# Performance work log

Hardware: AMD Instinct MI355X
Metric: run time of the kernel (lower is better)

The kernel has to match this reference:

```python
import jax, jax.numpy as jnp
import numpy as np

BETA = 0.025
K, D = 8192, 256
B, T = 32, 1024

def setup_inputs() -> dict:
    key = jax.random.key(0)
    k1, k2 = jax.random.split(key)
    z_e = jax.random.normal(k1, (B, T, D), dtype=jnp.float32)
    # variance_scaling(scale=1, mode='fan_avg', distribution='uniform') over (K, D)
    fan_avg = (K + D) / 2.0
    limit = np.sqrt(3.0 / fan_avg)
    codebook = jax.random.uniform(k2, (K, D), dtype=jnp.float32, minval=-limit, maxval=limit)
    return {"z_e": z_e, "codebook": codebook}

def reference(z_e, codebook):
    flat = z_e.reshape(-1, D)  # [N, D]
    x_sqr = jnp.sum(flat ** 2, axis=-1, keepdims=True)        # [N, 1]
    c_sqr = jnp.sum(codebook ** 2, axis=-1)[None, :]           # [1, K]
    distances = x_sqr - 2.0 * (flat @ codebook.T) + c_sqr      # [N, K]
    encoding_indices = jnp.argmin(distances, axis=-1).reshape(z_e.shape[:-1])  # [B, T]
    quantize = codebook[encoding_indices]                      # [B, T, D]
    encoding_loss = jnp.mean((jax.lax.stop_gradient(z_e) - quantize) ** 2)
    commitment_loss = jnp.mean((z_e - jax.lax.stop_gradient(quantize)) ** 2)
    loss = encoding_loss + BETA * commitment_loss
    z_q = z_e + jax.lax.stop_gradient(quantize - z_e)          # straight-through
    return (z_q, encoding_indices, loss)
```

## Files before the change

kernel.cpp:

```cpp
#include <hip/hip_runtime.h>

#define D     256
#define K     8192
#define NROWS 32768
#define BETA  0.025f
#define TAU_NEW 4e-4f
#define TAU_OLD 2e-4f

typedef __bf16 bf16x8 __attribute__((ext_vector_type(8)));
typedef unsigned short ushort8v __attribute__((ext_vector_type(8)));
typedef float f32x16 __attribute__((ext_vector_type(16)));

#define MFMA(a,b,c) __builtin_amdgcn_mfma_f32_32x32x16_bf16(a,b,c,0,0,0)

typedef __attribute__((address_space(3))) unsigned int lds_uint;
typedef __attribute__((address_space(1))) unsigned int glb_uint;
__device__ __forceinline__ void gld16(const void* g, void* l) {
    __builtin_amdgcn_global_load_lds((const glb_uint*)g, (lds_uint*)l, 16, 0, 0);
}

__device__ __forceinline__ unsigned short bf_rn(float x) {
    unsigned u = __float_as_uint(x);
    return (unsigned short)((u + 0x7FFFu + ((u >> 16) & 1u)) >> 16);
}
__device__ __forceinline__ void split2(float x, unsigned short& h, unsigned short& l) {
    h = bf_rn(x);
    float hf = __uint_as_float(((unsigned)h) << 16);
    l = bf_rn(x - hf);
}

__global__ __launch_bounds__(256)
void np_sumsq_kernel(const float* __restrict__ src, float* __restrict__ dst,
                     int nrows) {
    const int tid  = threadIdx.x;
    const int w    = tid >> 6;
    const int lane = tid & 63;
    const int row  = blockIdx.x * 4 + w;
    if (row >= nrows) return;
    const float* a = src + (size_t)row * D;
    float r = 0.0f;
    if (lane < 16) {
        const float* h = a + (lane >> 3) * 128;
        const int j = lane & 7;
        float v = h[j];
        r = __fmul_rn(v, v);
        #pragma unroll
        for (int i = 8; i < 128; i += 8) {
            float u = h[i + j];
            r = __fadd_rn(r, __fmul_rn(u, u));
        }
    }
    float rr[16];
    #pragma unroll
    for (int t = 0; t < 16; ++t) rr[t] = __shfl(r, t, 64);
    if (lane == 0) {
        float h0 = __fadd_rn(__fadd_rn(__fadd_rn(rr[0], rr[1]), __fadd_rn(rr[2], rr[3])),
                             __fadd_rn(__fadd_rn(rr[4], rr[5]), __fadd_rn(rr[6], rr[7])));
        float h1 = __fadd_rn(__fadd_rn(__fadd_rn(rr[8], rr[9]), __fadd_rn(rr[10], rr[11])),
                             __fadd_rn(__fadd_rn(rr[12], rr[13]), __fadd_rn(rr[14], rr[15])));
        dst[row] = __fadd_rn(h0, h1);
    }
}

__global__ __launch_bounds__(64)
void np_sumsq_flagged_kernel(const float* __restrict__ ze,
                             const int* __restrict__ nflag,
                             const int* __restrict__ flags,
                             float* __restrict__ x2, int cap) {
    const int lane = threadIdx.x;
    const int nf   = min(nflag[0], cap);
    for (int f = blockIdx.x; f < nf; f += gridDim.x) {
        const int row = flags[f];
        const float* a = ze + (size_t)row * D;
        float r = 0.0f;
        if (lane < 16) {
            const float* h = a + (lane >> 3) * 128;
            const int j = lane & 7;
            float v = h[j];
            r = __fmul_rn(v, v);
            #pragma unroll
            for (int i = 8; i < 128; i += 8) {
                float u = h[i + j];
                r = __fadd_rn(r, __fmul_rn(u, u));
            }
        }
        float rr[16];
        #pragma unroll
        for (int t = 0; t < 16; ++t) rr[t] = __shfl(r, t, 64);
        if (lane == 0) {
            float h0 = __fadd_rn(__fadd_rn(__fadd_rn(rr[0], rr[1]), __fadd_rn(rr[2], rr[3])),
                                 __fadd_rn(__fadd_rn(rr[4], rr[5]), __fadd_rn(rr[6], rr[7])));
            float h1 = __fadd_rn(__fadd_rn(__fadd_rn(rr[8], rr[9]), __fadd_rn(rr[10], rr[11])),
                                 __fadd_rn(__fadd_rn(rr[12], rr[13]), __fadd_rn(rr[14], rr[15])));
            x2[row] = __fadd_rn(h0, h1);
        }
    }
}

__global__ __launch_bounds__(256)
void pack_cb_kernel(const float* __restrict__ cb, unsigned short* __restrict__ cbp) {
    const int t  = blockIdx.x;
    const int l  = threadIdx.x & 63;
    const int cq = threadIdx.x >> 6;
    const int row = t * 32 + (l & 31);
    const int db  = 8 * (l >> 5);
    #pragma unroll
    for (int ci = 0; ci < 4; ++ci) {
        const int c  = cq * 4 + ci;
        const int d0 = c * 16 + db;
        float4 v0 = *reinterpret_cast<const float4*>(&cb[(size_t)row * D + d0]);
        float4 v1 = *reinterpret_cast<const float4*>(&cb[(size_t)row * D + d0 + 4]);
        float xv[8] = {v0.x, v0.y, v0.z, v0.w, v1.x, v1.y, v1.z, v1.w};
        ushort8v uh, ul;
        #pragma unroll
        for (int j = 0; j < 8; ++j) {
            unsigned short hh, ll;
            split2(xv[j], hh, ll);
            uh[j] = hh; ul[j] = ll;
        }
        *reinterpret_cast<ushort8v*>(cbp + (size_t)t * 16384 + (c * 2 + 0) * 512 + l * 8) = uh;
        *reinterpret_cast<ushort8v*>(cbp + (size_t)t * 16384 + (c * 2 + 1) * 512 + l * 8) = ul;
    }
}

__global__ __attribute__((amdgpu_waves_per_eu(2, 2))) __launch_bounds__(256)
void mfma_argmin_kernel(const float* __restrict__ ze,
                        const unsigned short* __restrict__ cbp,
                        const float* __restrict__ c2,
                        float2* __restrict__ tops, int* __restrict__ topi) {
    __shared__ unsigned short lds[2 * 16384];
    const int tid = threadIdx.x;
    const int l   = tid & 63;
    const int w   = tid >> 6;
    const int ks  = blockIdx.x & 1;
    const int nb  = blockIdx.x >> 1;
    const int n   = nb * 128 + w * 32 + (l & 31);
    const int h   = l >> 5;

    bf16x8 Bh[16], Bl[16];
    {
        const float* zr = ze + (size_t)n * D + 8 * h;
        #pragma unroll
        for (int c = 0; c < 16; ++c) {
            float4 v0 = *reinterpret_cast<const float4*>(zr + c * 16);
            float4 v1 = *reinterpret_cast<const float4*>(zr + c * 16 + 4);
            float xv[8] = {v0.x, v0.y, v0.z, v0.w, v1.x, v1.y, v1.z, v1.w};
            ushort8v uh, ul;
            #pragma unroll
            for (int j = 0; j < 8; ++j) {
                unsigned short hh, ll;
                split2(xv[j], hh, ll);
                uh[j] = hh; ul[j] = ll;
            }
            Bh[c] = __builtin_bit_cast(bf16x8, uh);
            Bl[c] = __builtin_bit_cast(bf16x8, ul);
        }
    }

    const int t0 = ks * 128;
    const uint4* gsrc = reinterpret_cast<const uint4*>(cbp);

    auto stage = [&](int t, int buf) {
        const uint4* g = gsrc + (size_t)t * 2048 + w * 512 + l;
        uint4* lb = reinterpret_cast<uint4*>(lds + buf * 16384) + w * 512;
        #pragma unroll
        for (int r = 0; r < 8; ++r)
            gld16(g + r * 64, lb + r * 64);
    };

    stage(t0, 0);
    __builtin_amdgcn_sched_barrier(0);
    __syncthreads();

    float b1 = 3.4e38f, b2 = 3.4e38f;
    int   i1 = 0;
    int   cur = 0;

    for (int ti = 0; ti < 128; ++ti) {
        const int t = t0 + ti;
        if (ti + 1 < 128) stage(t + 1, cur ^ 1);
        __builtin_amdgcn_sched_barrier(0);

        const uint4* abuf = reinterpret_cast<const uint4*>(lds + cur * 16384);
        f32x16 accA, accB;
        #pragma unroll
        for (int i = 0; i < 16; ++i) { accA[i] = 0.0f; accB[i] = 0.0f; }
        #pragma unroll
        for (int c = 0; c < 16; ++c) {
            bf16x8 Ah = __builtin_bit_cast(bf16x8, abuf[(c * 2 + 0) * 64 + l]);
            bf16x8 Al = __builtin_bit_cast(bf16x8, abuf[(c * 2 + 1) * 64 + l]);
            accA = MFMA(Ah, Bh[c], accA);
            accB = MFMA(Ah, Bl[c], accB);
            accB = MFMA(Al, Bh[c], accB);
        }
        const float* c2t = c2 + t * 32 + 4 * h;
        const int base = t * 32 + 4 * h;
        #pragma unroll
        for (int g = 0; g < 4; ++g) {
            float4 cv = *reinterpret_cast<const float4*>(c2t + 8 * g);
            #pragma unroll
            for (int q = 0; q < 4; ++q) {
                const int reg = g * 4 + q;
                float dot = accA[reg] + accB[reg];
                float cc  = (q == 0) ? cv.x : (q == 1) ? cv.y : (q == 2) ? cv.z : cv.w;
                float s   = fmaf(-2.0f, dot, cc);
                int code  = base + 8 * g + q;
                bool lt = s < b1;
                b2 = fminf(b2, lt ? b1 : s);
                i1 = lt ? code : i1;
                b1 = lt ? s : b1;
            }
        }
        __syncthreads();
        cur ^= 1;
    }

    float ob1 = __shfl_xor(b1, 32);
    float ob2 = __shfl_xor(b2, 32);
    int   oi1 = __shfl_xor(i1, 32);
    bool take = (ob1 < b1) || (ob1 == b1 && oi1 < i1);
    float nb2 = fminf(fmaxf(b1, ob1), fminf(b2, ob2));
    float nb1 = take ? ob1 : b1;
    int   ni1 = take ? oi1 : i1;
    if (l < 32) {
        tops[(size_t)n * 2 + ks] = make_float2(nb1, nb2);
        topi[(size_t)n * 2 + ks] = ni1;
    }
}

__global__ __launch_bounds__(256)
void ksplit_merge_kernel(const float2* __restrict__ tops, const int* __restrict__ topi,
                         int* __restrict__ idx_out, float* __restrict__ idxf_out,
                         int* __restrict__ nflag, int* __restrict__ flags, float tau) {
    const int n = blockIdx.x * 256 + threadIdx.x;
    float2 e0 = tops[(size_t)n * 2 + 0];
    float2 e1 = tops[(size_t)n * 2 + 1];
    int    i0 = topi[(size_t)n * 2 + 0];
    int    i1v = topi[(size_t)n * 2 + 1];
    bool take = (e1.x < e0.x) || (e1.x == e0.x && i1v < i0);
    float b1 = take ? e1.x : e0.x;
    int   bi = take ? i1v : i0;
    float b2 = fminf(fmaxf(e0.x, e1.x), fminf(e0.y, e1.y));
    idx_out[n]  = bi;
    idxf_out[n] = (float)bi;
    if (b2 - b1 < tau) {
        int p = atomicAdd(nflag, 1);
        flags[p] = n;
    }
}

__global__ __launch_bounds__(256)
void fix1_kernel(const float* __restrict__ ze, const float* __restrict__ cb,
                 const float* __restrict__ c2, const float* __restrict__ x2,
                 const int* __restrict__ nflag, const int* __restrict__ flags,
                 float* __restrict__ scr_s, int* __restrict__ scr_i, int cap) {
    __shared__ float sz[D];
    __shared__ float sbest[16];
    __shared__ int   sbi[16];
    const int tid  = threadIdx.x;
    const int cl   = tid >> 4;
    const int dt   = tid & 15;
    const int code = blockIdx.x * 16 + cl;
    const int nf   = min(nflag[0], cap);
    for (int f = 0; f < nf; ++f) {
        const int row = flags[f];
        __syncthreads();
        sz[tid] = ze[(size_t)row * D + tid];
        __syncthreads();
        double dot = 0.0;
        const float* cr = cb + (size_t)code * D + dt * 16;
        #pragma unroll
        for (int i = 0; i < 16; ++i)
            dot = fma((double)sz[dt * 16 + i], (double)cr[i], dot);
        #pragma unroll
        for (int o = 1; o < 16; o <<= 1)
            dot += __shfl_xor(dot, o);
        if (dt == 0) {
            float P  = (float)dot;
            float t3 = __fadd_rn(x2[row], __fmul_rn(-2.0f, P));
            float t4 = __fadd_rn(t3, c2[code]);
            sbest[cl] = t4; sbi[cl] = code;
        }
        __syncthreads();
        if (tid == 0) {
            float bs = sbest[0]; int bi = sbi[0];
            #pragma unroll
            for (int c = 1; c < 16; ++c)
                if (sbest[c] < bs) { bs = sbest[c]; bi = sbi[c]; }
            scr_s[(size_t)f * 512 + blockIdx.x] = bs;
            scr_i[(size_t)f * 512 + blockIdx.x] = bi;
        }
    }
}

__global__ __launch_bounds__(256)
void fix2_kernel(const int* __restrict__ nflag, const int* __restrict__ flags,
                 const float* __restrict__ scr_s, const int* __restrict__ scr_i,
                 int* __restrict__ idx_out, float* __restrict__ idxf_out, int cap) {
    __shared__ float ss[256];
    __shared__ int   si[256];
    const int tid = threadIdx.x;
    const int nf  = min(nflag[0], cap);
    for (int f = blockIdx.x; f < nf; f += gridDim.x) {
        float s0 = scr_s[(size_t)f * 512 + tid];
        int   j0 = scr_i[(size_t)f * 512 + tid];
        float s1 = scr_s[(size_t)f * 512 + 256 + tid];
        int   j1 = scr_i[(size_t)f * 512 + 256 + tid];
        bool take = (s1 < s0) || (s1 == s0 && j1 < j0);
        ss[tid] = take ? s1 : s0;
        si[tid] = take ? j1 : j0;
        __syncthreads();
        for (int o = 128; o; o >>= 1) {
            if (tid < o) {
                if (ss[tid + o] < ss[tid] ||
                    (ss[tid + o] == ss[tid] && si[tid + o] < si[tid])) {
                    ss[tid] = ss[tid + o]; si[tid] = si[tid + o];
                }
            }
            __syncthreads();
        }
        if (tid == 0) {
            const int row = flags[f];
            idx_out[row]  = si[0];
            idxf_out[row] = (float)si[0];
        }
        __syncthreads();
    }
}

__global__ __launch_bounds__(512)
void argmin_fp32_kernel(const float* __restrict__ ze, const float* __restrict__ cb,
                        const float* __restrict__ c2,
                        int* __restrict__ idx_out, float* __restrict__ idxf_out,
                        int* __restrict__ nflag, int* __restrict__ flags) {
    __shared__ float smem[12672];
    float* a_s = smem;
    float* b_s = smem + 32 * 128;
    const int tid  = threadIdx.x;
    const int tx   = tid & 31;
    const int ty   = tid >> 5;
    const int row0 = blockIdx.x * 128;
    float b1[8], b2[8];
    int   i1[8];
    #pragma unroll
    for (int r = 0; r < 8; ++r) { b1[r] = 3.4e38f; b2[r] = 3.4e38f; i1[r] = 0; }
    for (int kt = 0; kt < K; kt += 256) {
        float acc[8][8];
        #pragma unroll
        for (int r = 0; r < 8; ++r)
            #pragma unroll
            for (int c = 0; c < 8; ++c) acc[r][c] = 0.0f;
        for (int dc = 0; dc < D; dc += 32) {
            __syncthreads();
            #pragma unroll
            for (int j = 0; j < 2; ++j) {
                int p = tid + j * 512, ar = p >> 3, ad = (p & 7) << 2;
                float4 v = *reinterpret_cast<const float4*>(&ze[(size_t)(row0 + ar) * D + dc + ad]);
                a_s[(ad + 0) * 128 + ar] = v.x; a_s[(ad + 1) * 128 + ar] = v.y;
                a_s[(ad + 2) * 128 + ar] = v.z; a_s[(ad + 3) * 128 + ar] = v.w;
            }
            #pragma unroll
            for (int j = 0; j < 4; ++j) {
                int p = tid + j * 512, br = p >> 3, bd = (p & 7) << 2;
                float4 v = *reinterpret_cast<const float4*>(&cb[(size_t)(kt + br) * D + dc + bd]);
                b_s[(bd + 0) * 256 + br] = v.x; b_s[(bd + 1) * 256 + br] = v.y;
                b_s[(bd + 2) * 256 + br] = v.z; b_s[(bd + 3) * 256 + br] = v.w;
            }
            __syncthreads();
            #pragma unroll 4
            for (int d = 0; d < 32; ++d) {
                float4 a0  = *reinterpret_cast<const float4*>(&a_s[d * 128 + ty * 4]);
                float4 a1  = *reinterpret_cast<const float4*>(&a_s[d * 128 + 64 + ty * 4]);
                float4 b0  = *reinterpret_cast<const float4*>(&b_s[d * 256 + tx * 4]);
                float4 b1v = *reinterpret_cast<const float4*>(&b_s[d * 256 + 128 + tx * 4]);
                float av[8] = {a0.x, a0.y, a0.z, a0.w, a1.x, a1.y, a1.z, a1.w};
                float bv[8] = {b0.x, b0.y, b0.z, b0.w, b1v.x, b1v.y, b1v.z, b1v.w};
                #pragma unroll
                for (int r = 0; r < 8; ++r)
                    #pragma unroll
                    for (int c = 0; c < 8; ++c)
                        acc[r][c] = fmaf(av[r], bv[c], acc[r][c]);
            }
        }
        float4 cs0 = *reinterpret_cast<const float4*>(&c2[kt + tx * 4]);
        float4 cs1 = *reinterpret_cast<const float4*>(&c2[kt + 128 + tx * 4]);
        float cv[8] = {cs0.x, cs0.y, cs0.z, cs0.w, cs1.x, cs1.y, cs1.z, cs1.w};
        #pragma unroll
        for (int r = 0; r < 8; ++r)
            #pragma unroll
            for (int c = 0; c < 8; ++c) {
                int col = kt + ((c < 4) ? (tx * 4 + c) : (128 + tx * 4 + (c - 4)));
                float s = fmaf(-2.0f, acc[r][c], cv[c]);
                if (s < b1[r]) { b2[r] = b1[r]; b1[r] = s; i1[r] = col; }
                else if (s < b2[r]) { b2[r] = s; }
            }
    }
    __syncthreads();
    float* rs1 = smem;
    int*   ri  = (int*)(smem + 4224);
    float* rs2 = smem + 8448;
    #pragma unroll
    for (int r = 0; r < 8; ++r) {
        int lrow = (r >> 2) * 64 + ty * 4 + (r & 3);
        rs1[lrow * 33 + tx] = b1[r]; ri[lrow * 33 + tx] = i1[r]; rs2[lrow * 33 + tx] = b2[r];
    }
    __syncthreads();
    if (tid < 128) {
        float B1 = 3.4e38f, B2 = 3.4e38f;
        int I1 = 0;
        #pragma unroll 4
        for (int t = 0; t < 32; ++t) {
            float s1 = rs1[tid * 33 + t]; int j1 = ri[tid * 33 + t]; float s2 = rs2[tid * 33 + t];
            if (s1 < B1 || (s1 == B1 && j1 < I1)) { B2 = fminf(B2, B1); B1 = s1; I1 = j1; }
            else B2 = fminf(B2, s1);
            B2 = fminf(B2, s2);
        }
        int grow = row0 + tid;
        idx_out[grow] = I1;
        idxf_out[grow] = (float)I1;
        if (B2 - B1 < TAU_OLD) { int p = atomicAdd(nflag, 1); flags[p] = grow; }
    }
}

__global__ __launch_bounds__(256)
void fix_old_kernel(const float* __restrict__ ze, const float* __restrict__ cb,
                    const float* __restrict__ c2, const float* __restrict__ x2,
                    const int* __restrict__ nflag, const int* __restrict__ flags,
                    int* __restrict__ idx_out, float* __restrict__ idxf_out) {
    __shared__ __align__(16) float sx[D];
    __shared__ float sbest[256];
    __shared__ int   sidx[256];
    const int tid = threadIdx.x;
    const int n   = nflag[0];
    for (int f = blockIdx.x; f < n; f += gridDim.x) {
        __syncthreads();
        const int row = flags[f];
        sx[tid] = ze[(size_t)row * D + tid];
        const float x2r = x2[row];
        __syncthreads();
        const float4* sx4 = reinterpret_cast<const float4*>(sx);
        float best = 3.4e38f; int bi = K;
        for (int k = tid; k < K; k += 256) {
            const float4* cbr = reinterpret_cast<const float4*>(&cb[(size_t)k * D]);
            double dot = 0.0;
            #pragma unroll 8
            for (int d4 = 0; d4 < D / 4; ++d4) {
                float4 c = cbr[d4]; float4 x = sx4[d4];
                dot = fma((double)x.x, (double)c.x, dot);
                dot = fma((double)x.y, (double)c.y, dot);
                dot = fma((double)x.z, (double)c.z, dot);
                dot = fma((double)x.w, (double)c.w, dot);
            }
            float P  = (float)dot;
            float t3 = __fadd_rn(x2r, __fmul_rn(-2.0f, P));
            float t4 = __fadd_rn(t3, c2[k]);
            if (t4 < best || (t4 == best && k < bi)) { best = t4; bi = k; }
        }
        sbest[tid] = best; sidx[tid] = bi;
        __syncthreads();
        for (int o = 128; o; o >>= 1) {
            if (tid < o) {
                if (sbest[tid + o] < sbest[tid] ||
                    (sbest[tid + o] == sbest[tid] && sidx[tid + o] < sidx[tid])) {
                    sbest[tid] = sbest[tid + o]; sidx[tid] = sidx[tid + o];
                }
            }
            __syncthreads();
        }
        if (tid == 0) { idx_out[row] = sidx[0]; idxf_out[row] = (float)sidx[0]; }
    }
}

__global__ __launch_bounds__(256)
void gather_loss_kernel(const float* __restrict__ ze, const float* __restrict__ cb,
                        const int* __restrict__ idx, float* __restrict__ zq,
                        float* __restrict__ partial) {
    const int tid  = threadIdx.x;
    const int w    = tid >> 6;
    const int lane = tid & 63;
    const int n    = blockIdx.x * 4 + w;
    const int k    = idx[n];
    float4 q = *reinterpret_cast<const float4*>(&cb[(size_t)k * D + lane * 4]);
    float4 z = *reinterpret_cast<const float4*>(&ze[(size_t)n * D + lane * 4]);
    *reinterpret_cast<float4*>(&zq[(size_t)n * D + lane * 4]) = q;
    float dx = z.x - q.x, dy = z.y - q.y, dz = z.z - q.z, dw = z.w - q.w;
    float s = dx * dx + dy * dy + dz * dz + dw * dw;
    #pragma unroll
    for (int o = 32; o; o >>= 1) s += __shfl_down(s, o);
    __shared__ float ws4[4];
    if (lane == 0) ws4[w] = s;
    __syncthreads();
    if (tid == 0) partial[blockIdx.x] = ws4[0] + ws4[1] + ws4[2] + ws4[3];
}

__global__ __launch_bounds__(256)
void final_loss_kernel(const float* __restrict__ partial, float* __restrict__ out) {
    __shared__ float sm[256];
    const int tid = threadIdx.x;
    float s = 0.0f;
    for (int i = tid; i < 8192; i += 256) s += partial[i];
    sm[tid] = s;
    __syncthreads();
    #pragma unroll
    for (int o = 128; o; o >>= 1) {
        if (tid < o) sm[tid] += sm[tid + o];
        __syncthreads();
    }
    if (tid == 0)
        out[0] = sm[0] * (1.0f + BETA) / (float)(NROWS * D);
}

extern "C" void kernel_launch(void* const* d_in, const int* in_sizes, int n_in,
                              void* d_out, int out_size, void* d_ws, size_t ws_size,
                              hipStream_t stream) {
    const float* ze = (const float*)d_in[0];
    const float* cb = (const float*)d_in[1];

    float* out  = (float*)d_out;
    float* zq   = out;
    float* idxf = out + (size_t)NROWS * D;
    float* loss = out + (size_t)NROWS * D + NROWS;

    char* ws = (char*)d_ws;
    float*  c2      = (float*) (ws);
    float*  x2      = (float*) (ws + 32768);
    int*    idx     = (int*)   (ws + 163840);
    float*  partial = (float*) (ws + 294912);
    int*    nflag   = (int*)   (ws + 327680);
    int*    flags   = (int*)   (ws + 327696);
    float2* tops    = (float2*)(ws + 458768);
    int*    topi    = (int*)   (ws + 983056);
    unsigned short* cbp = (unsigned short*)(ws + 1245200);
    float*  scr_s   = (float*) (ws + 9633808);
    const size_t scr_base = 9633808;

    const size_t need_min = scr_base + (size_t)2048 * 4096;
    const bool newpath = ws_size >= need_min;
    int cap = 0;
    int* scr_i = nullptr;
    if (newpath) {
        size_t avail = (ws_size - scr_base) / 4096;
        cap = (int)(avail > 8192 ? 8192 : avail);
        scr_i = (int*)(ws + scr_base + (size_t)cap * 2048);
    }

    hipMemsetAsync(nflag, 0, sizeof(int), stream);
    hipLaunchKernelGGL(np_sumsq_kernel, dim3(K / 4), dim3(256), 0, stream, cb, c2, K);

    if (newpath) {
        hipLaunchKernelGGL(pack_cb_kernel,     dim3(256), dim3(256), 0, stream, cb, cbp);
        hipLaunchKernelGGL(mfma_argmin_kernel, dim3(512), dim3(256), 0, stream,
                           ze, cbp, c2, tops, topi);
        hipLaunchKernelGGL(ksplit_merge_kernel, dim3(NROWS / 256), dim3(256), 0, stream,
                           tops, topi, idx, idxf, nflag, flags, TAU_NEW);
        hipLaunchKernelGGL(np_sumsq_flagged_kernel, dim3(128), dim3(64), 0, stream,
                           ze, nflag, flags, x2, cap);
        hipLaunchKernelGGL(fix1_kernel, dim3(512), dim3(256), 0, stream,
                           ze, cb, c2, x2, nflag, flags, scr_s, scr_i, cap);
        hipLaunchKernelGGL(fix2_kernel, dim3(64), dim3(256), 0, stream,
                           nflag, flags, scr_s, scr_i, idx, idxf, cap);
    } else {
        hipLaunchKernelGGL(argmin_fp32_kernel, dim3(NROWS / 128), dim3(512), 0, stream,
                           ze, cb, c2, idx, idxf, nflag, flags);
        hipLaunchKernelGGL(np_sumsq_flagged_kernel, dim3(128), dim3(64), 0, stream,
                           ze, nflag, flags, x2, NROWS);
        hipLaunchKernelGGL(fix_old_kernel, dim3(256), dim3(256), 0, stream,
                           ze, cb, c2, x2, nflag, flags, idx, idxf);
    }

    hipLaunchKernelGGL(gather_loss_kernel, dim3(NROWS / 4), dim3(256), 0, stream,
                       ze, cb, idx, zq, partial);
    hipLaunchKernelGGL(final_loss_kernel, dim3(1), dim3(256), 0, stream,
                       partial, loss);
}
```

Before: 522.2 us.

## Switch argmin GEMM to 16x16x32 MFMA with 8 waves per block

Replaces the 32x32x16 bf16 MFMA tiling with 16x16x32 MFMAs, repacks the codebook layout to match, and doubles the block to 512 threads (8 waves, 16 rows each). It also changes the per-tile top-2 argmin update into a small pairwise tree reduction, and adds a two-step cross-lane merge at the end. The goal is more waves in flight and a shorter serial compare chain. The cost is more MFMA instructions per tile and a lower per-wave register budget under the new launch bounds.

```diff
diff --git a/kernel.cpp b/kernel.cpp
--- a/kernel.cpp
+++ b/kernel.cpp
@@ -9,9 +9,9 @@
 
 typedef __bf16 bf16x8 __attribute__((ext_vector_type(8)));
 typedef unsigned short ushort8v __attribute__((ext_vector_type(8)));
-typedef float f32x16 __attribute__((ext_vector_type(16)));
-
-#define MFMA(a,b,c) __builtin_amdgcn_mfma_f32_32x32x16_bf16(a,b,c,0,0,0)
+typedef float f32x4 __attribute__((ext_vector_type(4)));
+
+#define MFMA16(a,b,c) __builtin_amdgcn_mfma_f32_16x16x32_bf16(a,b,c,0,0,0)
 
 typedef __attribute__((address_space(3))) unsigned int lds_uint;
 typedef __attribute__((address_space(1))) unsigned int glb_uint;
@@ -99,31 +99,35 @@
 
 __global__ __launch_bounds__(256)
 void pack_cb_kernel(const float* __restrict__ cb, unsigned short* __restrict__ cbp) {
-    const int t  = blockIdx.x;
-    const int l  = threadIdx.x & 63;
-    const int cq = threadIdx.x >> 6;
-    const int row = t * 32 + (l & 31);
-    const int db  = 8 * (l >> 5);
+    const int t = blockIdx.x;
+    const int l = threadIdx.x & 63;
+    const int q = threadIdx.x >> 6;
+    const int h = l >> 4;
     #pragma unroll
-    for (int ci = 0; ci < 4; ++ci) {
-        const int c  = cq * 4 + ci;
-        const int d0 = c * 16 + db;
-        float4 v0 = *reinterpret_cast<const float4*>(&cb[(size_t)row * D + d0]);
-        float4 v1 = *reinterpret_cast<const float4*>(&cb[(size_t)row * D + d0 + 4]);
-        float xv[8] = {v0.x, v0.y, v0.z, v0.w, v1.x, v1.y, v1.z, v1.w};
-        ushort8v uh, ul;
-        #pragma unroll
-        for (int j = 0; j < 8; ++j) {
-            unsigned short hh, ll;
-            split2(xv[j], hh, ll);
-            uh[j] = hh; ul[j] = ll;
-        }
-        *reinterpret_cast<ushort8v*>(cbp + (size_t)t * 16384 + (c * 2 + 0) * 512 + l * 8) = uh;
-        *reinterpret_cast<ushort8v*>(cbp + (size_t)t * 16384 + (c * 2 + 1) * 512 + l * 8) = ul;
-    }
-}
-
-__global__ __attribute__((amdgpu_waves_per_eu(2, 2))) __launch_bounds__(256)
+    for (int ci = 0; ci < 2; ++ci) {
+        const int c = q * 2 + ci;
+        #pragma unroll
+        for (int cs = 0; cs < 2; ++cs) {
+            const int code = t * 32 + cs * 16 + (l & 15);
+            const int d0   = c * 32 + 8 * h;
+            float4 v0 = *reinterpret_cast<const float4*>(&cb[(size_t)code * D + d0]);
+            float4 v1 = *reinterpret_cast<const float4*>(&cb[(size_t)code * D + d0 + 4]);
+            float xv[8] = {v0.x, v0.y, v0.z, v0.w, v1.x, v1.y, v1.z, v1.w};
+            ushort8v uh, ul;
+            #pragma unroll
+            for (int j = 0; j < 8; ++j) {
+                unsigned short hh, ll;
+                split2(xv[j], hh, ll);
+                uh[j] = hh; ul[j] = ll;
+            }
+            const size_t base = (((size_t)t * 8 + c) * 2 + cs) * 2;
+            *reinterpret_cast<ushort8v*>(cbp + (base + 0) * 512 + l * 8) = uh;
+            *reinterpret_cast<ushort8v*>(cbp + (base + 1) * 512 + l * 8) = ul;
+        }
+    }
+}
+
+__global__ __launch_bounds__(512)
 void mfma_argmin_kernel(const float* __restrict__ ze,
                         const unsigned short* __restrict__ cbp,
                         const float* __restrict__ c2,
@@ -134,16 +138,16 @@
     const int w   = tid >> 6;
     const int ks  = blockIdx.x & 1;
     const int nb  = blockIdx.x >> 1;
-    const int n   = nb * 128 + w * 32 + (l & 31);
-    const int h   = l >> 5;
-
-    bf16x8 Bh[16], Bl[16];
+    const int n   = nb * 128 + w * 16 + (l & 15);
+    const int h   = l >> 4;
+
+    bf16x8 Bh[8], Bl[8];
     {
         const float* zr = ze + (size_t)n * D + 8 * h;
         #pragma unroll
-        for (int c = 0; c < 16; ++c) {
-            float4 v0 = *reinterpret_cast<const float4*>(zr + c * 16);
-            float4 v1 = *reinterpret_cast<const float4*>(zr + c * 16 + 4);
+        for (int c = 0; c < 8; ++c) {
+            float4 v0 = *reinterpret_cast<const float4*>(zr + c * 32);
+            float4 v1 = *reinterpret_cast<const float4*>(zr + c * 32 + 4);
             float xv[8] = {v0.x, v0.y, v0.z, v0.w, v1.x, v1.y, v1.z, v1.w};
             ushort8v uh, ul;
             #pragma unroll
@@ -161,11 +165,13 @@
     const uint4* gsrc = reinterpret_cast<const uint4*>(cbp);
 
     auto stage = [&](int t, int buf) {
-        const uint4* g = gsrc + (size_t)t * 2048 + w * 512 + l;
-        uint4* lb = reinterpret_cast<uint4*>(lds + buf * 16384) + w * 512;
-        #pragma unroll
-        for (int r = 0; r < 8; ++r)
-            gld16(g + r * 64, lb + r * 64);
+        const uint4* gbase = gsrc + (size_t)t * 2048;
+        uint4* lbase = reinterpret_cast<uint4*>(lds + buf * 16384);
+        #pragma unroll
+        for (int r = 0; r < 4; ++r) {
+            const int idx = r * 512 + w * 64;
+            gld16(gbase + idx + l, lbase + idx);
+        }
     };
 
     stage(t0, 0);
@@ -182,49 +188,83 @@
         __builtin_amdgcn_sched_barrier(0);
 
         const uint4* abuf = reinterpret_cast<const uint4*>(lds + cur * 16384);
-        f32x16 accA, accB;
-        #pragma unroll
-        for (int i = 0; i < 16; ++i) { accA[i] = 0.0f; accB[i] = 0.0f; }
-        #pragma unroll
-        for (int c = 0; c < 16; ++c) {
-            bf16x8 Ah = __builtin_bit_cast(bf16x8, abuf[(c * 2 + 0) * 64 + l]);
-            bf16x8 Al = __builtin_bit_cast(bf16x8, abuf[(c * 2 + 1) * 64 + l]);
-            accA = MFMA(Ah, Bh[c], accA);
-            accB = MFMA(Ah, Bl[c], accB);
-            accB = MFMA(Al, Bh[c], accB);
-        }
-        const float* c2t = c2 + t * 32 + 4 * h;
-        const int base = t * 32 + 4 * h;
-        #pragma unroll
-        for (int g = 0; g < 4; ++g) {
-            float4 cv = *reinterpret_cast<const float4*>(c2t + 8 * g);
-            #pragma unroll
-            for (int q = 0; q < 4; ++q) {
-                const int reg = g * 4 + q;
-                float dot = accA[reg] + accB[reg];
-                float cc  = (q == 0) ? cv.x : (q == 1) ? cv.y : (q == 2) ? cv.z : cv.w;
-                float s   = fmaf(-2.0f, dot, cc);
-                int code  = base + 8 * g + q;
-                bool lt = s < b1;
-                b2 = fminf(b2, lt ? b1 : s);
-                i1 = lt ? code : i1;
-                b1 = lt ? s : b1;
-            }
-        }
+        f32x4 accA[2], accB[2];
+        #pragma unroll
+        for (int cs = 0; cs < 2; ++cs)
+            #pragma unroll
+            for (int i = 0; i < 4; ++i) { accA[cs][i] = 0.0f; accB[cs][i] = 0.0f; }
+
+        #pragma unroll
+        for (int c = 0; c < 8; ++c) {
+            #pragma unroll
+            for (int cs = 0; cs < 2; ++cs) {
+                bf16x8 Ah = __builtin_bit_cast(bf16x8, abuf[((c * 2 + cs) * 2 + 0) * 64 + l]);
+                bf16x8 Al = __builtin_bit_cast(bf16x8, abuf[((c * 2 + cs) * 2 + 1) * 64 + l]);
+                accA[cs] = MFMA16(Ah, Bh[c], accA[cs]);
+                accB[cs] = MFMA16(Ah, Bl[c], accB[cs]);
+                accB[cs] = MFMA16(Al, Bh[c], accB[cs]);
+            }
+        }
+
+        float s[8];
+        #pragma unroll
+        for (int cs = 0; cs < 2; ++cs) {
+            const int base = t * 32 + cs * 16 + h * 4;
+            float4 cv = *reinterpret_cast<const float4*>(c2 + base);
+            #pragma unroll
+            for (int r = 0; r < 4; ++r) {
+                float dot = accA[cs][r] + accB[cs][r];
+                float cc  = (r == 0) ? cv.x : (r == 1) ? cv.y : (r == 2) ? cv.z : cv.w;
+                s[cs * 4 + r] = fmaf(-2.0f, dot, cc);
+            }
+        }
+        float m1[4], m2[4]; int ix[4];
+        #pragma unroll
+        for (int p = 0; p < 4; ++p) {
+            const int codeA = t * 32 + (p >> 1) * 16 + h * 4 + (p & 1) * 2;
+            float sa = s[2 * p], sb = s[2 * p + 1];
+            bool bl = sb < sa;
+            m1[p] = bl ? sb : sa;
+            m2[p] = bl ? sa : sb;
+            ix[p] = codeA + (bl ? 1 : 0);
+        }
+        #pragma unroll
+        for (int step = 1; step < 4; step <<= 1) {
+            #pragma unroll
+            for (int i = 0; i < 4; i += 2 * step) {
+                const int a = i, b = i + step;
+                float t2 = fminf(m2[a], m2[b]);
+                bool bl = m1[b] < m1[a];
+                float lose = bl ? m1[a] : m1[b];
+                m2[a] = fminf(t2, lose);
+                m1[a] = bl ? m1[b] : m1[a];
+                ix[a] = bl ? ix[b] : ix[a];
+            }
+        }
+        {
+            bool lt = m1[0] < b1;
+            b2 = fminf(fminf(b2, m2[0]), lt ? b1 : m1[0]);
+            i1 = lt ? ix[0] : i1;
+            b1 = lt ? m1[0] : b1;
+        }
+
         __syncthreads();
         cur ^= 1;
     }
 
-    float ob1 = __shfl_xor(b1, 32);
-    float ob2 = __shfl_xor(b2, 32);
-    int   oi1 = __shfl_xor(i1, 32);
-    bool take = (ob1 < b1) || (ob1 == b1 && oi1 < i1);
-    float nb2 = fminf(fmaxf(b1, ob1), fminf(b2, ob2));
-    float nb1 = take ? ob1 : b1;
-    int   ni1 = take ? oi1 : i1;
-    if (l < 32) {
-        tops[(size_t)n * 2 + ks] = make_float2(nb1, nb2);
-        topi[(size_t)n * 2 + ks] = ni1;
+    #pragma unroll
+    for (int mask = 16; mask <= 32; mask <<= 1) {
+        float os1 = __shfl_xor(b1, mask);
+        float os2 = __shfl_xor(b2, mask);
+        int   oi  = __shfl_xor(i1, mask);
+        bool take = (os1 < b1) || (os1 == b1 && oi < i1);
+        b2 = fminf(fmaxf(b1, os1), fminf(b2, os2));
+        b1 = take ? os1 : b1;
+        i1 = take ? oi  : i1;
+    }
+    if (l < 16) {
+        tops[(size_t)n * 2 + ks] = make_float2(b1, b2);
+        topi[(size_t)n * 2 + ks] = i1;
     }
 }
 
@@ -549,7 +589,7 @@
 
     if (newpath) {
         hipLaunchKernelGGL(pack_cb_kernel,     dim3(256), dim3(256), 0, stream, cb, cbp);
-        hipLaunchKernelGGL(mfma_argmin_kernel, dim3(512), dim3(256), 0, stream,
+        hipLaunchKernelGGL(mfma_argmin_kernel, dim3(512), dim3(512), 0, stream,
                            ze, cbp, c2, tops, topi);
         hipLaunchKernelGGL(ksplit_merge_kernel, dim3(NROWS / 256), dim3(256), 0, stream,
                            tops, topi, idx, idxf, nflag, flags, TAU_NEW);
```

New measurement: 518.8 us. Within noise of the previous version (-0.6%).

## Switch argmin GEMM from split-bf16 to single fp16 MFMA and parallelize fix pass

Applied to the files above, without the earlier changes.

Replaces the three-MFMA split-bf16 distance computation with one fp16 MFMA per chunk, which halves the packed codebook size and LDS staging and cuts matrix work to a third. Since fp16 is less accurate, the near-tie threshold is raised so more rows go to the exact fp64 fix pass. The fix kernel is restriped over the flagged rows with many more blocks to absorb the larger flagged set. The risks are many more flagged rows and fp16 range or precision problems with the inputs.

```diff
diff --git a/kernel.cpp b/kernel.cpp
--- a/kernel.cpp
+++ b/kernel.cpp
@@ -4,29 +4,19 @@
 #define K     8192
 #define NROWS 32768
 #define BETA  0.025f
-#define TAU_NEW 4e-4f
+#define TAU_NEW 2e-3f
 #define TAU_OLD 2e-4f
 
-typedef __bf16 bf16x8 __attribute__((ext_vector_type(8)));
+typedef _Float16 f16x8 __attribute__((ext_vector_type(8)));
 typedef unsigned short ushort8v __attribute__((ext_vector_type(8)));
 typedef float f32x16 __attribute__((ext_vector_type(16)));
 
-#define MFMA(a,b,c) __builtin_amdgcn_mfma_f32_32x32x16_bf16(a,b,c,0,0,0)
+#define MFMAH(a,b,c) __builtin_amdgcn_mfma_f32_32x32x16_f16(a,b,c,0,0,0)
 
 typedef __attribute__((address_space(3))) unsigned int lds_uint;
 typedef __attribute__((address_space(1))) unsigned int glb_uint;
 __device__ __forceinline__ void gld16(const void* g, void* l) {
     __builtin_amdgcn_global_load_lds((const glb_uint*)g, (lds_uint*)l, 16, 0, 0);
-}
-
-__device__ __forceinline__ unsigned short bf_rn(float x) {
-    unsigned u = __float_as_uint(x);
-    return (unsigned short)((u + 0x7FFFu + ((u >> 16) & 1u)) >> 16);
-}
-__device__ __forceinline__ void split2(float x, unsigned short& h, unsigned short& l) {
-    h = bf_rn(x);
-    float hf = __uint_as_float(((unsigned)h) << 16);
-    l = bf_rn(x - hf);
 }
 
 __global__ __launch_bounds__(256)
@@ -111,24 +101,19 @@
         float4 v0 = *reinterpret_cast<const float4*>(&cb[(size_t)row * D + d0]);
         float4 v1 = *reinterpret_cast<const float4*>(&cb[(size_t)row * D + d0 + 4]);
         float xv[8] = {v0.x, v0.y, v0.z, v0.w, v1.x, v1.y, v1.z, v1.w};
-        ushort8v uh, ul;
-        #pragma unroll
-        for (int j = 0; j < 8; ++j) {
-            unsigned short hh, ll;
-            split2(xv[j], hh, ll);
-            uh[j] = hh; ul[j] = ll;
-        }
-        *reinterpret_cast<ushort8v*>(cbp + (size_t)t * 16384 + (c * 2 + 0) * 512 + l * 8) = uh;
-        *reinterpret_cast<ushort8v*>(cbp + (size_t)t * 16384 + (c * 2 + 1) * 512 + l * 8) = ul;
-    }
-}
-
-__global__ __attribute__((amdgpu_waves_per_eu(2, 2))) __launch_bounds__(256)
+        f16x8 hv;
+        #pragma unroll
+        for (int j = 0; j < 8; ++j) hv[j] = (_Float16)xv[j];
+        *reinterpret_cast<f16x8*>(cbp + (((size_t)t * 16 + c) * 64 + l) * 8) = hv;
+    }
+}
+
+__global__ __launch_bounds__(256)
 void mfma_argmin_kernel(const float* __restrict__ ze,
                         const unsigned short* __restrict__ cbp,
                         const float* __restrict__ c2,
                         float2* __restrict__ tops, int* __restrict__ topi) {
-    __shared__ unsigned short lds[2 * 16384];
+    __shared__ unsigned short lds[2 * 8192];
     const int tid = threadIdx.x;
     const int l   = tid & 63;
     const int w   = tid >> 6;
@@ -137,7 +122,7 @@
     const int n   = nb * 128 + w * 32 + (l & 31);
     const int h   = l >> 5;
 
-    bf16x8 Bh[16], Bl[16];
+    f16x8 Bf[16];
     {
         const float* zr = ze + (size_t)n * D + 8 * h;
         #pragma unroll
@@ -145,15 +130,10 @@
             float4 v0 = *reinterpret_cast<const float4*>(zr + c * 16);
             float4 v1 = *reinterpret_cast<const float4*>(zr + c * 16 + 4);
             float xv[8] = {v0.x, v0.y, v0.z, v0.w, v1.x, v1.y, v1.z, v1.w};
-            ushort8v uh, ul;
-            #pragma unroll
-            for (int j = 0; j < 8; ++j) {
-                unsigned short hh, ll;
-                split2(xv[j], hh, ll);
-                uh[j] = hh; ul[j] = ll;
-            }
-            Bh[c] = __builtin_bit_cast(bf16x8, uh);
-            Bl[c] = __builtin_bit_cast(bf16x8, ul);
+            f16x8 hv;
+            #pragma unroll
+            for (int j = 0; j < 8; ++j) hv[j] = (_Float16)xv[j];
+            Bf[c] = hv;
         }
     }
 
@@ -161,10 +141,10 @@
     const uint4* gsrc = reinterpret_cast<const uint4*>(cbp);
 
     auto stage = [&](int t, int buf) {
-        const uint4* g = gsrc + (size_t)t * 2048 + w * 512 + l;
-        uint4* lb = reinterpret_cast<uint4*>(lds + buf * 16384) + w * 512;
-        #pragma unroll
-        for (int r = 0; r < 8; ++r)
+        const uint4* g = gsrc + (size_t)t * 1024 + w * 256 + l;
+        uint4* lb = reinterpret_cast<uint4*>(lds + buf * 8192) + w * 256;
+        #pragma unroll
+        for (int r = 0; r < 4; ++r)
             gld16(g + r * 64, lb + r * 64);
     };
 
@@ -181,17 +161,16 @@
         if (ti + 1 < 128) stage(t + 1, cur ^ 1);
         __builtin_amdgcn_sched_barrier(0);
 
-        const uint4* abuf = reinterpret_cast<const uint4*>(lds + cur * 16384);
-        f32x16 accA, accB;
-        #pragma unroll
-        for (int i = 0; i < 16; ++i) { accA[i] = 0.0f; accB[i] = 0.0f; }
-        #pragma unroll
-        for (int c = 0; c < 16; ++c) {
-            bf16x8 Ah = __builtin_bit_cast(bf16x8, abuf[(c * 2 + 0) * 64 + l]);
-            bf16x8 Al = __builtin_bit_cast(bf16x8, abuf[(c * 2 + 1) * 64 + l]);
-            accA = MFMA(Ah, Bh[c], accA);
-            accB = MFMA(Ah, Bl[c], accB);
-            accB = MFMA(Al, Bh[c], accB);
+        const uint4* abuf = reinterpret_cast<const uint4*>(lds + cur * 8192);
+        f32x16 a0, a1;
+        #pragma unroll
+        for (int i = 0; i < 16; ++i) { a0[i] = 0.0f; a1[i] = 0.0f; }
+        #pragma unroll
+        for (int c = 0; c < 16; c += 2) {
+            f16x8 A0 = __builtin_bit_cast(f16x8, abuf[(c + 0) * 64 + l]);
+            f16x8 A1 = __builtin_bit_cast(f16x8, abuf[(c + 1) * 64 + l]);
+            a0 = MFMAH(A0, Bf[c + 0], a0);
+            a1 = MFMAH(A1, Bf[c + 1], a1);
         }
         const float* c2t = c2 + t * 32 + 4 * h;
         const int base = t * 32 + 4 * h;
@@ -201,7 +180,7 @@
             #pragma unroll
             for (int q = 0; q < 4; ++q) {
                 const int reg = g * 4 + q;
-                float dot = accA[reg] + accB[reg];
+                float dot = a0[reg] + a1[reg];
                 float cc  = (q == 0) ? cv.x : (q == 1) ? cv.y : (q == 2) ? cv.z : cv.w;
                 float s   = fmaf(-2.0f, dot, cc);
                 int code  = base + 8 * g + q;
@@ -257,12 +236,15 @@
     __shared__ float sz[D];
     __shared__ float sbest[16];
     __shared__ int   sbi[16];
-    const int tid  = threadIdx.x;
-    const int cl   = tid >> 4;
-    const int dt   = tid & 15;
-    const int code = blockIdx.x * 16 + cl;
-    const int nf   = min(nflag[0], cap);
-    for (int f = 0; f < nf; ++f) {
+    const int tid     = threadIdx.x;
+    const int cl      = tid >> 4;
+    const int dt      = tid & 15;
+    const int cbblk   = blockIdx.x & 511;
+    const int stripe  = blockIdx.x >> 9;
+    const int nstripe = gridDim.x >> 9;
+    const int code    = cbblk * 16 + cl;
+    const int nf      = min(nflag[0], cap);
+    for (int f = stripe; f < nf; f += nstripe) {
         const int row = flags[f];
         __syncthreads();
         sz[tid] = ze[(size_t)row * D + tid];
@@ -287,8 +269,8 @@
             #pragma unroll
             for (int c = 1; c < 16; ++c)
                 if (sbest[c] < bs) { bs = sbest[c]; bi = sbi[c]; }
-            scr_s[(size_t)f * 512 + blockIdx.x] = bs;
-            scr_i[(size_t)f * 512 + blockIdx.x] = bi;
+            scr_s[(size_t)f * 512 + cbblk] = bs;
+            scr_i[(size_t)f * 512 + cbblk] = bi;
         }
     }
 }
@@ -553,11 +535,11 @@
                            ze, cbp, c2, tops, topi);
         hipLaunchKernelGGL(ksplit_merge_kernel, dim3(NROWS / 256), dim3(256), 0, stream,
                            tops, topi, idx, idxf, nflag, flags, TAU_NEW);
-        hipLaunchKernelGGL(np_sumsq_flagged_kernel, dim3(128), dim3(64), 0, stream,
+        hipLaunchKernelGGL(np_sumsq_flagged_kernel, dim3(256), dim3(64), 0, stream,
                            ze, nflag, flags, x2, cap);
-        hipLaunchKernelGGL(fix1_kernel, dim3(512), dim3(256), 0, stream,
+        hipLaunchKernelGGL(fix1_kernel, dim3(8192), dim3(256), 0, stream,
                            ze, cb, c2, x2, nflag, flags, scr_s, scr_i, cap);
-        hipLaunchKernelGGL(fix2_kernel, dim3(64), dim3(256), 0, stream,
+        hipLaunchKernelGGL(fix2_kernel, dim3(128), dim3(256), 0, stream,
                            nflag, flags, scr_s, scr_i, idx, idxf, cap);
     } else {
         hipLaunchKernelGGL(argmin_fp32_kernel, dim3(NROWS / 128), dim3(512), 0, stream,
```

Result: faster. 507.3 us (-2.9%).
